# Kernel tuning notes

Hardware: AMD Instinct MI355X
Metric: run time of the kernel (lower is better)

The kernel has to match this reference:

```python
import jax, jax.numpy as jnp
import numpy as np

B, S, C, HD = 2, 4096, 2048, 128
H = C // HD  # 16 heads
EPS = 1.1920929e-07  # torch RMSNorm default eps for float32 (finfo.eps)


def _make_rope(seq_len, head_dim):
    # Standard RoPE 2x2 rotation matrices: [1, S, 1, head_dim//2, 2, 2]
    half = head_dim // 2
    freqs = 1.0 / (10000.0 ** (np.arange(0, half, dtype=np.float32) / half))
    ang = np.arange(seq_len, dtype=np.float32)[:, None] * freqs[None, :]  # [S, half]
    cos, sin = np.cos(ang), np.sin(ang)
    rot = np.stack([np.stack([cos, -sin], axis=-1),
                    np.stack([sin, cos], axis=-1)], axis=-2)  # [S, half, 2, 2]
    return jnp.asarray(rot[None, :, None])  # [1, S, 1, half, 2, 2]


def setup_inputs() -> dict:
    key = jax.random.key(0)
    ks = jax.random.split(key, 9)
    sc = 1.0 / np.sqrt(C)
    return {
        "x": jax.random.normal(ks[0], (B, S, C), jnp.float32),
        "rope": _make_rope(S, HD),
        "wq": jax.random.normal(ks[1], (C, C), jnp.float32) * sc,
        "bq": jax.random.normal(ks[2], (C,), jnp.float32) * 0.01,
        "wk": jax.random.normal(ks[3], (C, C), jnp.float32) * sc,
        "bk": jax.random.normal(ks[4], (C,), jnp.float32) * 0.01,
        "wv": jax.random.normal(ks[5], (C, C), jnp.float32) * sc,
        "bv": jax.random.normal(ks[6], (C,), jnp.float32) * 0.01,
        "q_norm_w": jnp.ones((HD,), jnp.float32),
        "k_norm_w": jnp.ones((HD,), jnp.float32),
    }


def _rmsnorm(t, w):
    t32 = t.astype(jnp.float32)
    inv = jax.lax.rsqrt(jnp.mean(t32 * t32, axis=-1, keepdims=True) + EPS)
    return (t32 * inv * w).astype(t.dtype)


def _apply_rotary(t, rope):
    # t: [B, S, H, HD] -> pairs [B, S, H, HD//2, 1, 2]; rope: [1, S, 1, HD//2, 2, 2]
    t32 = t.reshape(*t.shape[:-1], HD // 2, 1, 2).astype(jnp.float32)
    out = (rope * t32).sum(axis=-1)  # [B, S, H, HD//2, 2]
    return out.reshape(t.shape).astype(t.dtype)


def reference(x, rope, wq, bq, wk, bk, wv, bv, q_norm_w, k_norm_w):
    # QKV projections (torch Linear: x @ W^T + b)
    q = (jnp.einsum('bsc,oc->bso', x, wq) + bq).reshape(B, S, H, HD)
    k = (jnp.einsum('bsc,oc->bso', x, wk) + bk).reshape(B, S, H, HD)
    v = (jnp.einsum('bsc,oc->bso', x, wv) + bv).reshape(B, S, H, HD)
    # Per-head RMSNorm on q, k (in float32, cast back), then rotary
    q = _apply_rotary(_rmsnorm(q, q_norm_w), rope)
    k = _apply_rotary(_rmsnorm(k, k_norm_w), rope)
    return (q, k, v)
```

## Files before the change

kernel.cpp:

```cpp
#include <hip/hip_runtime.h>


#define M_DIM 8192
#define N_DIM 6144
#define K_DIM 2048
#define NKT 32
#define EPS_RMS 1.1920929e-07f

typedef __bf16 bf16x8 __attribute__((ext_vector_type(8)));
typedef float f32x4 __attribute__((ext_vector_type(4)));

__device__ __forceinline__ void gload16(const void* g, void* l) {
  __builtin_amdgcn_global_load_lds(
      (const __attribute__((address_space(1))) unsigned int*)g,
      (__attribute__((address_space(3))) unsigned int*)l, 16, 0, 0);
}

__device__ __forceinline__ unsigned short f2bf(float f) {
  union { float f; unsigned u; } x; x.f = f;
  unsigned r = x.u + 0x7FFFu + ((x.u >> 16) & 1u);
  return (unsigned short)(r >> 16);
}

__global__ void __launch_bounds__(256) cvt_all(
    const float* __restrict__ x, const float* __restrict__ wq,
    const float* __restrict__ wk, const float* __restrict__ wv,
    unsigned short* __restrict__ xbf, unsigned short* __restrict__ wbf) {
  const int nx4 = M_DIM * K_DIM / 4;
  const int nw4 = K_DIM * K_DIM / 4;
  const int tot = nx4 + 3 * nw4;
  int i = blockIdx.x * blockDim.x + threadIdx.x;
  const int stride = gridDim.x * blockDim.x;
  for (; i < tot; i += stride) {
    const float* s;
    unsigned short* d;
    int j;
    if (i < nx4) { s = x; d = xbf; j = i; }
    else {
      const int k = i - nx4;
      const int sel = k / nw4;
      j = k - sel * nw4;
      s = sel == 0 ? wq : (sel == 1 ? wk : wv);
      d = wbf + (size_t)sel * K_DIM * K_DIM;
    }
    const float4 v = reinterpret_cast<const float4*>(s)[j];
    ushort4 o;
    o.x = f2bf(v.x); o.y = f2bf(v.y); o.z = f2bf(v.z); o.w = f2bf(v.w);
    reinterpret_cast<ushort4*>(d)[j] = o;
  }
}

#define LDS4(ARR, BASE, OFF) (*(const f32x4*)((const char*)(ARR) + (BASE) + (OFF)))

#define SGB_DS(N)   __builtin_amdgcn_sched_group_barrier(0x100, (N), 0)
#define SGB_MFMA(N) __builtin_amdgcn_sched_group_barrier(0x8, (N), 0)

#define MFMA_PH(MH, NH)                                                              \
  {                                                                                  \
    _Pragma("unroll")                                                                \
    for (int mf4 = 0; mf4 < 4; ++mf4) {                                              \
      _Pragma("unroll")                                                              \
      for (int nf2 = 0; nf2 < 2; ++nf2) {                                            \
        f32x4& c = acc[(MH) * 4 + mf4][(NH) * 2 + nf2];                              \
        c = __builtin_amdgcn_mfma_f32_16x16x32_bf16(                                 \
            __builtin_bit_cast(bf16x8, Af[mf4][0]),                                  \
            __builtin_bit_cast(bf16x8, Bf[NH][nf2][0]), c, 0, 0, 0);                 \
        c = __builtin_amdgcn_mfma_f32_16x16x32_bf16(                                 \
            __builtin_bit_cast(bf16x8, Af[mf4][1]),                                  \
            __builtin_bit_cast(bf16x8, Bf[NH][nf2][1]), c, 0, 0, 0);                 \
      }                                                                              \
    }                                                                                \
  }

#define FENCE asm volatile("" ::: "memory")

__global__ void __launch_bounds__(512, 2) gemm_fused(
    const unsigned short* __restrict__ xbf, const unsigned short* __restrict__ wbf,
    const float* __restrict__ rope,
    const float* __restrict__ bq, const float* __restrict__ bk, const float* __restrict__ bv,
    const float* __restrict__ qnw, const float* __restrict__ knw,
    float* __restrict__ dout) {
  const int id = blockIdx.x;
  const int xcd = id & 7;
  const int jb = id >> 3;
  const int bm = (xcd << 2) | (jb & 3);
  const int bn = jb >> 2;
  const int m0 = bm << 8, n0 = bn << 8;
  const int tid = threadIdx.x;
  const int w = tid >> 6, l = tid & 63;
  const int l15 = l & 15, lhi = l >> 4;
  const int wr = w >> 2, wc = w & 3;

  __shared__ __align__(16) unsigned short As[32768];
  __shared__ __align__(16) unsigned short Bs[32768];

  const int srow = tid >> 3;
  const int schunk = (tid & 7) ^ (srow & 7);
  const unsigned short* aSrc = xbf + ((size_t)(m0 + srow) << 11) + (schunk << 3);
  const unsigned short* bSrc = wbf + ((size_t)(n0 + srow) << 11) + (schunk << 3);
  char* aDst = (char*)As + (w << 10);
  char* bDst = (char*)Bs + (w << 10);

#define STA(KT, Q) gload16(aSrc + ((size_t)(Q) << 17) + ((KT) << 6), aDst + ((((KT) & 1) << 15) + ((Q) << 13)))
#define STB(KT, Q) gload16(bSrc + ((size_t)(Q) << 17) + ((KT) << 6), bDst + ((((KT) & 1) << 15) + ((Q) << 13)))

  const int sl0 = ((lhi ^ (l15 & 7)) << 4);
  const int sl1 = (((lhi + 4) ^ (l15 & 7)) << 4);
  unsigned a0 = (wr << 14) + (l15 << 7) + sl0;
  unsigned a1 = (wr << 14) + (l15 << 7) + sl1;
  unsigned b0 = (wc << 13) + (l15 << 7) + sl0;
  unsigned b1 = (wc << 13) + (l15 << 7) + sl1;

  f32x4 acc[8][4];
#pragma unroll
  for (int i = 0; i < 8; ++i)
#pragma unroll
    for (int jj = 0; jj < 4; ++jj) acc[i][jj] = (f32x4){0.f, 0.f, 0.f, 0.f};

  f32x4 Af[4][2];
  f32x4 Bf[2][2][2];

  STA(0, 0); STA(0, 2);
  STB(0, 0); STB(0, 1); STB(0, 2); STB(0, 3);
  STA(0, 1); STA(0, 3);
  asm volatile("s_waitcnt vmcnt(2)" ::: "memory");
  __builtin_amdgcn_s_barrier();
  FENCE;

  for (int kt = 0; kt < NKT; ++kt) {
    const bool notLast = (kt < NKT - 1);
    Af[0][0] = LDS4(As, a0, 0);        Af[0][1] = LDS4(As, a1, 0);
    Bf[0][0][0] = LDS4(Bs, b0, 0);     Bf[0][0][1] = LDS4(Bs, b1, 0);
    Bf[0][1][0] = LDS4(Bs, b0, 2048);  Bf[0][1][1] = LDS4(Bs, b1, 2048);
    Af[1][0] = LDS4(As, a0, 2048);     Af[1][1] = LDS4(As, a1, 2048);
    Af[2][0] = LDS4(As, a0, 4096);     Af[2][1] = LDS4(As, a1, 4096);
    Af[3][0] = LDS4(As, a0, 6144);     Af[3][1] = LDS4(As, a1, 6144);
    Bf[1][0][0] = LDS4(Bs, b0, 4096);  Bf[1][0][1] = LDS4(Bs, b1, 4096);
    Bf[1][1][0] = LDS4(Bs, b0, 6144);  Bf[1][1][1] = LDS4(Bs, b1, 6144);
    if (notLast) {
      STA(kt + 1, 0); STA(kt + 1, 2);
      STB(kt + 1, 0); STB(kt + 1, 1); STB(kt + 1, 2); STB(kt + 1, 3);
    }
    __builtin_amdgcn_s_setprio(1);
    MFMA_PH(0, 0);
    MFMA_PH(0, 1);
    SGB_DS(4);  SGB_MFMA(2);
    SGB_DS(2);  SGB_MFMA(2);
    SGB_DS(2);  SGB_MFMA(4);
    SGB_DS(2);  SGB_MFMA(4);
    SGB_DS(2);  SGB_MFMA(4);
    SGB_DS(4);  SGB_MFMA(16);
    __builtin_amdgcn_s_setprio(0);
    if (notLast) { asm volatile("s_waitcnt vmcnt(6)" ::: "memory"); }
    else         { asm volatile("s_waitcnt vmcnt(0)" ::: "memory"); }
    __builtin_amdgcn_s_barrier();
    FENCE;
    Af[0][0] = LDS4(As, a0, 8192);  Af[0][1] = LDS4(As, a1, 8192);
    Af[1][0] = LDS4(As, a0, 10240); Af[1][1] = LDS4(As, a1, 10240);
    Af[2][0] = LDS4(As, a0, 12288); Af[2][1] = LDS4(As, a1, 12288);
    Af[3][0] = LDS4(As, a0, 14336); Af[3][1] = LDS4(As, a1, 14336);
    if (notLast) { STA(kt + 1, 1); STA(kt + 1, 3); }
    __builtin_amdgcn_s_setprio(1);
    MFMA_PH(1, 0);
    MFMA_PH(1, 1);
    SGB_DS(2);  SGB_MFMA(4);
    SGB_DS(2);  SGB_MFMA(4);
    SGB_DS(2);  SGB_MFMA(4);
    SGB_DS(2);  SGB_MFMA(4);
    SGB_MFMA(16);
    __builtin_amdgcn_s_setprio(0);
    if (notLast) { asm volatile("s_waitcnt vmcnt(2)" ::: "memory"); }
    __builtin_amdgcn_s_barrier();
    FENCE;
    a0 ^= 32768u; a1 ^= 32768u; b0 ^= 32768u; b1 ^= 32768u;
  }

  float* scr = (float*)As;
  const int sec = bn >> 3;
  const int nsec = (n0 & 2047) + (wc << 6);
  const float* bias = sec == 0 ? bq : (sec == 1 ? bk : bv);
  float biasv[4];
#pragma unroll
  for (int nf = 0; nf < 4; ++nf) biasv[nf] = bias[nsec + nf * 16 + l15];
  const size_t outBase = ((size_t)sec << 24);

  if (sec < 2) {
    const float* nwp = sec ? knw : qnw;
    const int colh = (wc & 1) << 6;
    float nwv[4];
#pragma unroll
    for (int nf = 0; nf < 4; ++nf) nwv[nf] = nwp[colh + nf * 16 + l15];
    float ssv[8][4];
#pragma unroll
    for (int mf = 0; mf < 8; ++mf) {
#pragma unroll
      for (int jj = 0; jj < 4; ++jj) {
        float ss = 0.f;
#pragma unroll
        for (int nf = 0; nf < 4; ++nf) {
          const float t = acc[mf][nf][jj] + biasv[nf];
          ss += t * t;
        }
        ss += __shfl_xor(ss, 1);
        ss += __shfl_xor(ss, 2);
        ss += __shfl_xor(ss, 4);
        ss += __shfl_xor(ss, 8);
        ssv[mf][jj] = ss;
      }
    }
    if (l15 == 0) {
#pragma unroll
      for (int mf = 0; mf < 8; ++mf)
#pragma unroll
        for (int jj = 0; jj < 4; ++jj)
          scr[(w << 7) + mf * 16 + (lhi << 2) + jj] = ssv[mf][jj];
    }
    __syncthreads();
#pragma unroll
    for (int mf = 0; mf < 8; ++mf) {
#pragma unroll
      for (int jj = 0; jj < 4; ++jj) {
        const float tot = ssv[mf][jj] + scr[((w ^ 1) << 7) + mf * 16 + (lhi << 2) + jj];
        const float inv = rsqrtf(tot * (1.0f / 128.0f) + EPS_RMS);
        const int m = m0 + (wr << 7) + mf * 16 + (lhi << 2) + jj;
        const float* rp = rope + ((size_t)(m & 4095) << 8);
        float* orow = dout + outBase + ((size_t)m << 11) + nsec + l15;
#pragma unroll
        for (int nf = 0; nf < 4; ++nf) {
          const float tn = (acc[mf][nf][jj] + biasv[nf]) * inv * nwv[nf];
          const float pn = __shfl_xor(tn, 1);
          const int ch = colh + nf * 16 + l15;
          const int jr = ch >> 1;
          const float o = fmaf(rp[jr << 2], tn, rp[(jr << 2) + 1 + (ch & 1)] * pn);
          orow[nf << 4] = o;
        }
      }
    }
  } else {
#pragma unroll
    for (int mf = 0; mf < 8; ++mf)
#pragma unroll
      for (int jj = 0; jj < 4; ++jj) {
        const int m = m0 + (wr << 7) + mf * 16 + (lhi << 2) + jj;
        float* orow = dout + outBase + ((size_t)m << 11) + nsec + l15;
#pragma unroll
        for (int nf = 0; nf < 4; ++nf) orow[nf << 4] = acc[mf][nf][jj] + biasv[nf];
      }
  }
}

extern "C" void kernel_launch(void* const* d_in, const int* in_sizes, int n_in,
                              void* d_out, int out_size, void* d_ws, size_t ws_size,
                              hipStream_t stream) {
  const float* x = (const float*)d_in[0];
  const float* rope = (const float*)d_in[1];
  const float* wq = (const float*)d_in[2];
  const float* bq = (const float*)d_in[3];
  const float* wk = (const float*)d_in[4];
  const float* bk = (const float*)d_in[5];
  const float* wv = (const float*)d_in[6];
  const float* bv = (const float*)d_in[7];
  const float* qnw = (const float*)d_in[8];
  const float* knw = (const float*)d_in[9];

  unsigned short* xbf = (unsigned short*)d_ws;
  unsigned short* wbf = xbf + (size_t)M_DIM * K_DIM;

  cvt_all<<<2048, 256, 0, stream>>>(x, wq, wk, wv, xbf, wbf);

  gemm_fused<<<(M_DIM / 256) * (N_DIM / 256), 512, 0, stream>>>(
      xbf, wbf, rope, bq, bk, bv, qnw, knw, (float*)d_out);
}
```

Baseline: 234.1 us.

## Split GEMM tile across 16 waves with 64x64 per-wave subtiles

Doubles the block to 1024 threads so each of 16 waves computes a 64x64 subtile of the unchanged 256x256 block tile, using 16 MFMA accumulators instead of 32. The LDS staging layout changes to two K-halves of 32 elements with a new swizzle, and the epilogue indexing is adjusted to match. The aim is more waves to hide latency and lower per-wave register pressure. In exchange, each wave reuses fewer loaded operands per MFMA, so LDS read traffic rises. The launch-bounds hint may also squeeze the VGPR budget enough to cause spills.

```diff
diff --git a/kernel.cpp b/kernel.cpp
--- a/kernel.cpp
+++ b/kernel.cpp
@@ -55,26 +55,22 @@
 #define SGB_DS(N)   __builtin_amdgcn_sched_group_barrier(0x100, (N), 0)
 #define SGB_MFMA(N) __builtin_amdgcn_sched_group_barrier(0x8, (N), 0)
 
-#define MFMA_PH(MH, NH)                                                              \
+#define MFMA_KS()                                                                    \
   {                                                                                  \
     _Pragma("unroll")                                                                \
-    for (int mf4 = 0; mf4 < 4; ++mf4) {                                              \
+    for (int mf = 0; mf < 4; ++mf) {                                                 \
       _Pragma("unroll")                                                              \
-      for (int nf2 = 0; nf2 < 2; ++nf2) {                                            \
-        f32x4& c = acc[(MH) * 4 + mf4][(NH) * 2 + nf2];                              \
-        c = __builtin_amdgcn_mfma_f32_16x16x32_bf16(                                 \
-            __builtin_bit_cast(bf16x8, Af[mf4][0]),                                  \
-            __builtin_bit_cast(bf16x8, Bf[NH][nf2][0]), c, 0, 0, 0);                 \
-        c = __builtin_amdgcn_mfma_f32_16x16x32_bf16(                                 \
-            __builtin_bit_cast(bf16x8, Af[mf4][1]),                                  \
-            __builtin_bit_cast(bf16x8, Bf[NH][nf2][1]), c, 0, 0, 0);                 \
+      for (int nf = 0; nf < 4; ++nf) {                                               \
+        acc[mf][nf] = __builtin_amdgcn_mfma_f32_16x16x32_bf16(                       \
+            __builtin_bit_cast(bf16x8, Af[mf]),                                      \
+            __builtin_bit_cast(bf16x8, Bf[nf]), acc[mf][nf], 0, 0, 0);               \
       }                                                                              \
     }                                                                                \
   }
 
 #define FENCE asm volatile("" ::: "memory")
 
-__global__ void __launch_bounds__(512, 2) gemm_fused(
+__global__ void __launch_bounds__(1024, 4) gemm_fused(
     const unsigned short* __restrict__ xbf, const unsigned short* __restrict__ wbf,
     const float* __restrict__ rope,
     const float* __restrict__ bq, const float* __restrict__ bk, const float* __restrict__ bv,
@@ -94,85 +90,66 @@
   __shared__ __align__(16) unsigned short As[32768];
   __shared__ __align__(16) unsigned short Bs[32768];
 
-  const int srow = tid >> 3;
-  const int schunk = (tid & 7) ^ (srow & 7);
-  const unsigned short* aSrc = xbf + ((size_t)(m0 + srow) << 11) + (schunk << 3);
-  const unsigned short* bSrc = wbf + ((size_t)(n0 + srow) << 11) + (schunk << 3);
+  const int srow = tid >> 2;
+  const int sch = (tid & 3) ^ ((tid >> 3) & 3);
+  const unsigned short* aSrc = xbf + ((size_t)(m0 + srow) << 11) + (sch << 3);
+  const unsigned short* bSrc = wbf + ((size_t)(n0 + srow) << 11) + (sch << 3);
   char* aDst = (char*)As + (w << 10);
   char* bDst = (char*)Bs + (w << 10);
 
-#define STA(KT, Q) gload16(aSrc + ((size_t)(Q) << 17) + ((KT) << 6), aDst + ((((KT) & 1) << 15) + ((Q) << 13)))
-#define STB(KT, Q) gload16(bSrc + ((size_t)(Q) << 17) + ((KT) << 6), bDst + ((((KT) & 1) << 15) + ((Q) << 13)))
-
-  const int sl0 = ((lhi ^ (l15 & 7)) << 4);
-  const int sl1 = (((lhi + 4) ^ (l15 & 7)) << 4);
-  unsigned a0 = (wr << 14) + (l15 << 7) + sl0;
-  unsigned a1 = (wr << 14) + (l15 << 7) + sl1;
-  unsigned b0 = (wc << 13) + (l15 << 7) + sl0;
-  unsigned b1 = (wc << 13) + (l15 << 7) + sl1;
-
-  f32x4 acc[8][4];
-#pragma unroll
-  for (int i = 0; i < 8; ++i)
+#define STAK(KT, KS) gload16(aSrc + ((KT) << 6) + ((KS) << 5), aDst + ((((KT) & 1) << 15) + ((KS) << 14)))
+#define STBK(KT, KS) gload16(bSrc + ((KT) << 6) + ((KS) << 5), bDst + ((((KT) & 1) << 15) + ((KS) << 14)))
+
+  const int slot = lhi ^ ((l15 >> 1) & 3);
+  unsigned aRd = (wr << 12) + (l15 << 6) + (slot << 4);
+  unsigned bRd = (wc << 12) + (l15 << 6) + (slot << 4);
+
+  f32x4 acc[4][4];
+#pragma unroll
+  for (int i = 0; i < 4; ++i)
 #pragma unroll
     for (int jj = 0; jj < 4; ++jj) acc[i][jj] = (f32x4){0.f, 0.f, 0.f, 0.f};
 
-  f32x4 Af[4][2];
-  f32x4 Bf[2][2][2];
-
-  STA(0, 0); STA(0, 2);
-  STB(0, 0); STB(0, 1); STB(0, 2); STB(0, 3);
-  STA(0, 1); STA(0, 3);
+  f32x4 Af[4], Bf[4];
+
+  STAK(0, 0); STBK(0, 0);
+  STAK(0, 1); STBK(0, 1);
   asm volatile("s_waitcnt vmcnt(2)" ::: "memory");
   __builtin_amdgcn_s_barrier();
   FENCE;
 
   for (int kt = 0; kt < NKT; ++kt) {
-    const bool notLast = (kt < NKT - 1);
-    Af[0][0] = LDS4(As, a0, 0);        Af[0][1] = LDS4(As, a1, 0);
-    Bf[0][0][0] = LDS4(Bs, b0, 0);     Bf[0][0][1] = LDS4(Bs, b1, 0);
-    Bf[0][1][0] = LDS4(Bs, b0, 2048);  Bf[0][1][1] = LDS4(Bs, b1, 2048);
-    Af[1][0] = LDS4(As, a0, 2048);     Af[1][1] = LDS4(As, a1, 2048);
-    Af[2][0] = LDS4(As, a0, 4096);     Af[2][1] = LDS4(As, a1, 4096);
-    Af[3][0] = LDS4(As, a0, 6144);     Af[3][1] = LDS4(As, a1, 6144);
-    Bf[1][0][0] = LDS4(Bs, b0, 4096);  Bf[1][0][1] = LDS4(Bs, b1, 4096);
-    Bf[1][1][0] = LDS4(Bs, b0, 6144);  Bf[1][1][1] = LDS4(Bs, b1, 6144);
-    if (notLast) {
-      STA(kt + 1, 0); STA(kt + 1, 2);
-      STB(kt + 1, 0); STB(kt + 1, 1); STB(kt + 1, 2); STB(kt + 1, 3);
-    }
+    const bool nl = (kt < NKT - 1);
+    Af[0] = LDS4(As, aRd, 0);    Bf[0] = LDS4(Bs, bRd, 0);
+    Af[1] = LDS4(As, aRd, 1024); Bf[1] = LDS4(Bs, bRd, 1024);
+    Af[2] = LDS4(As, aRd, 2048); Bf[2] = LDS4(Bs, bRd, 2048);
+    Af[3] = LDS4(As, aRd, 3072); Bf[3] = LDS4(Bs, bRd, 3072);
+    if (nl) { STAK(kt + 1, 0); STBK(kt + 1, 0); }
     __builtin_amdgcn_s_setprio(1);
-    MFMA_PH(0, 0);
-    MFMA_PH(0, 1);
-    SGB_DS(4);  SGB_MFMA(2);
-    SGB_DS(2);  SGB_MFMA(2);
-    SGB_DS(2);  SGB_MFMA(4);
-    SGB_DS(2);  SGB_MFMA(4);
-    SGB_DS(2);  SGB_MFMA(4);
-    SGB_DS(4);  SGB_MFMA(16);
+    MFMA_KS();
+    SGB_DS(4); SGB_MFMA(2);
+    SGB_DS(2); SGB_MFMA(1);
+    SGB_DS(2); SGB_MFMA(13);
     __builtin_amdgcn_s_setprio(0);
-    if (notLast) { asm volatile("s_waitcnt vmcnt(6)" ::: "memory"); }
-    else         { asm volatile("s_waitcnt vmcnt(0)" ::: "memory"); }
+    if (nl) { asm volatile("s_waitcnt vmcnt(2)" ::: "memory"); }
+    else    { asm volatile("s_waitcnt vmcnt(0)" ::: "memory"); }
     __builtin_amdgcn_s_barrier();
     FENCE;
-    Af[0][0] = LDS4(As, a0, 8192);  Af[0][1] = LDS4(As, a1, 8192);
-    Af[1][0] = LDS4(As, a0, 10240); Af[1][1] = LDS4(As, a1, 10240);
-    Af[2][0] = LDS4(As, a0, 12288); Af[2][1] = LDS4(As, a1, 12288);
-    Af[3][0] = LDS4(As, a0, 14336); Af[3][1] = LDS4(As, a1, 14336);
-    if (notLast) { STA(kt + 1, 1); STA(kt + 1, 3); }
+    Af[0] = LDS4(As, aRd, 16384); Bf[0] = LDS4(Bs, bRd, 16384);
+    Af[1] = LDS4(As, aRd, 17408); Bf[1] = LDS4(Bs, bRd, 17408);
+    Af[2] = LDS4(As, aRd, 18432); Bf[2] = LDS4(Bs, bRd, 18432);
+    Af[3] = LDS4(As, aRd, 19456); Bf[3] = LDS4(Bs, bRd, 19456);
+    if (nl) { STAK(kt + 1, 1); STBK(kt + 1, 1); }
     __builtin_amdgcn_s_setprio(1);
-    MFMA_PH(1, 0);
-    MFMA_PH(1, 1);
-    SGB_DS(2);  SGB_MFMA(4);
-    SGB_DS(2);  SGB_MFMA(4);
-    SGB_DS(2);  SGB_MFMA(4);
-    SGB_DS(2);  SGB_MFMA(4);
-    SGB_MFMA(16);
+    MFMA_KS();
+    SGB_DS(4); SGB_MFMA(2);
+    SGB_DS(2); SGB_MFMA(1);
+    SGB_DS(2); SGB_MFMA(13);
     __builtin_amdgcn_s_setprio(0);
-    if (notLast) { asm volatile("s_waitcnt vmcnt(2)" ::: "memory"); }
+    if (nl) { asm volatile("s_waitcnt vmcnt(2)" ::: "memory"); }
     __builtin_amdgcn_s_barrier();
     FENCE;
-    a0 ^= 32768u; a1 ^= 32768u; b0 ^= 32768u; b1 ^= 32768u;
+    aRd ^= 32768u; bRd ^= 32768u;
   }
 
   float* scr = (float*)As;
@@ -190,9 +167,9 @@
     float nwv[4];
 #pragma unroll
     for (int nf = 0; nf < 4; ++nf) nwv[nf] = nwp[colh + nf * 16 + l15];
-    float ssv[8][4];
-#pragma unroll
-    for (int mf = 0; mf < 8; ++mf) {
+    float ssv[4][4];
+#pragma unroll
+    for (int mf = 0; mf < 4; ++mf) {
 #pragma unroll
       for (int jj = 0; jj < 4; ++jj) {
         float ss = 0.f;
@@ -210,19 +187,19 @@
     }
     if (l15 == 0) {
 #pragma unroll
-      for (int mf = 0; mf < 8; ++mf)
+      for (int mf = 0; mf < 4; ++mf)
 #pragma unroll
         for (int jj = 0; jj < 4; ++jj)
-          scr[(w << 7) + mf * 16 + (lhi << 2) + jj] = ssv[mf][jj];
+          scr[(w << 6) + (mf << 4) + (lhi << 2) + jj] = ssv[mf][jj];
     }
     __syncthreads();
 #pragma unroll
-    for (int mf = 0; mf < 8; ++mf) {
+    for (int mf = 0; mf < 4; ++mf) {
 #pragma unroll
       for (int jj = 0; jj < 4; ++jj) {
-        const float tot = ssv[mf][jj] + scr[((w ^ 1) << 7) + mf * 16 + (lhi << 2) + jj];
+        const float tot = ssv[mf][jj] + scr[((w ^ 1) << 6) + (mf << 4) + (lhi << 2) + jj];
         const float inv = rsqrtf(tot * (1.0f / 128.0f) + EPS_RMS);
-        const int m = m0 + (wr << 7) + mf * 16 + (lhi << 2) + jj;
+        const int m = m0 + (wr << 6) + (mf << 4) + (lhi << 2) + jj;
         const float* rp = rope + ((size_t)(m & 4095) << 8);
         float* orow = dout + outBase + ((size_t)m << 11) + nsec + l15;
 #pragma unroll
@@ -238,10 +215,10 @@
     }
   } else {
 #pragma unroll
-    for (int mf = 0; mf < 8; ++mf)
+    for (int mf = 0; mf < 4; ++mf)
 #pragma unroll
       for (int jj = 0; jj < 4; ++jj) {
-        const int m = m0 + (wr << 7) + mf * 16 + (lhi << 2) + jj;
+        const int m = m0 + (wr << 6) + (mf << 4) + (lhi << 2) + jj;
         float* orow = dout + outBase + ((size_t)m << 11) + nsec + l15;
 #pragma unroll
         for (int nf = 0; nf < 4; ++nf) orow[nf << 4] = acc[mf][nf][jj] + biasv[nf];
@@ -268,6 +245,6 @@
 
   cvt_all<<<2048, 256, 0, stream>>>(x, wq, wk, wv, xbf, wbf);
 
-  gemm_fused<<<(M_DIM / 256) * (N_DIM / 256), 512, 0, stream>>>(
+  gemm_fused<<<(M_DIM / 256) * (N_DIM / 256), 1024, 0, stream>>>(
       xbf, wbf, rope, bq, bk, bv, qnw, knw, (float*)d_out);
 }
```

Result: slower. 242.6 us (+3.7%).

## Restructure GEMM main loop into four barrier-separated MFMA phases

Applied to the files above, without the earlier changes.

Replaces the two-phase main loop, which relied on sched_group_barrier interleaving, with four phases. Each phase issues its LDS fragment reads and part of the next-tile global-to-LDS loads, then does a block barrier, a full lgkmcnt wait and a sched_barrier before its MFMA block. Global loads for the next K tile are spread across the phases and B is issued before A. The aim is a ping-pong style schedule with more even overlap of memory and MFMA work, at the cost of extra barriers per K iteration and the loss of fine-grained compiler interleaving.

```diff
diff --git a/kernel.cpp b/kernel.cpp
--- a/kernel.cpp
+++ b/kernel.cpp
@@ -52,9 +52,6 @@
 
 #define LDS4(ARR, BASE, OFF) (*(const f32x4*)((const char*)(ARR) + (BASE) + (OFF)))
 
-#define SGB_DS(N)   __builtin_amdgcn_sched_group_barrier(0x100, (N), 0)
-#define SGB_MFMA(N) __builtin_amdgcn_sched_group_barrier(0x8, (N), 0)
-
 #define MFMA_PH(MH, NH)                                                              \
   {                                                                                  \
     _Pragma("unroll")                                                                \
@@ -73,6 +70,15 @@
   }
 
 #define FENCE asm volatile("" ::: "memory")
+
+#define PHASE_MFMA(MH, NH)                          \
+  FENCE;                                            \
+  __builtin_amdgcn_s_barrier();                     \
+  asm volatile("s_waitcnt lgkmcnt(0)" ::: "memory");\
+  __builtin_amdgcn_sched_barrier(0);                \
+  __builtin_amdgcn_s_setprio(1);                    \
+  MFMA_PH(MH, NH);                                  \
+  __builtin_amdgcn_s_setprio(0);
 
 __global__ void __launch_bounds__(512, 2) gemm_fused(
     const unsigned short* __restrict__ xbf, const unsigned short* __restrict__ wbf,
@@ -120,56 +126,41 @@
   f32x4 Af[4][2];
   f32x4 Bf[2][2][2];
 
+  STB(0, 0); STB(0, 1); STB(0, 2); STB(0, 3);
   STA(0, 0); STA(0, 2);
-  STB(0, 0); STB(0, 1); STB(0, 2); STB(0, 3);
   STA(0, 1); STA(0, 3);
   asm volatile("s_waitcnt vmcnt(2)" ::: "memory");
   __builtin_amdgcn_s_barrier();
   FENCE;
 
   for (int kt = 0; kt < NKT; ++kt) {
-    const bool notLast = (kt < NKT - 1);
+    const bool nl = (kt < NKT - 1);
     Af[0][0] = LDS4(As, a0, 0);        Af[0][1] = LDS4(As, a1, 0);
-    Bf[0][0][0] = LDS4(Bs, b0, 0);     Bf[0][0][1] = LDS4(Bs, b1, 0);
-    Bf[0][1][0] = LDS4(Bs, b0, 2048);  Bf[0][1][1] = LDS4(Bs, b1, 2048);
     Af[1][0] = LDS4(As, a0, 2048);     Af[1][1] = LDS4(As, a1, 2048);
     Af[2][0] = LDS4(As, a0, 4096);     Af[2][1] = LDS4(As, a1, 4096);
     Af[3][0] = LDS4(As, a0, 6144);     Af[3][1] = LDS4(As, a1, 6144);
+    Bf[0][0][0] = LDS4(Bs, b0, 0);     Bf[0][0][1] = LDS4(Bs, b1, 0);
+    Bf[0][1][0] = LDS4(Bs, b0, 2048);  Bf[0][1][1] = LDS4(Bs, b1, 2048);
+    if (nl) { STB(kt + 1, 0); STB(kt + 1, 1); }
+    PHASE_MFMA(0, 0);
+    __builtin_amdgcn_s_barrier();
     Bf[1][0][0] = LDS4(Bs, b0, 4096);  Bf[1][0][1] = LDS4(Bs, b1, 4096);
     Bf[1][1][0] = LDS4(Bs, b0, 6144);  Bf[1][1][1] = LDS4(Bs, b1, 6144);
-    if (notLast) {
-      STA(kt + 1, 0); STA(kt + 1, 2);
-      STB(kt + 1, 0); STB(kt + 1, 1); STB(kt + 1, 2); STB(kt + 1, 3);
-    }
-    __builtin_amdgcn_s_setprio(1);
-    MFMA_PH(0, 0);
-    MFMA_PH(0, 1);
-    SGB_DS(4);  SGB_MFMA(2);
-    SGB_DS(2);  SGB_MFMA(2);
-    SGB_DS(2);  SGB_MFMA(4);
-    SGB_DS(2);  SGB_MFMA(4);
-    SGB_DS(2);  SGB_MFMA(4);
-    SGB_DS(4);  SGB_MFMA(16);
-    __builtin_amdgcn_s_setprio(0);
-    if (notLast) { asm volatile("s_waitcnt vmcnt(6)" ::: "memory"); }
-    else         { asm volatile("s_waitcnt vmcnt(0)" ::: "memory"); }
-    __builtin_amdgcn_s_barrier();
-    FENCE;
+    if (nl) { STB(kt + 1, 2); STB(kt + 1, 3); }
+    PHASE_MFMA(0, 1);
+    if (nl) { asm volatile("s_waitcnt vmcnt(4)" ::: "memory"); }
+    else    { asm volatile("s_waitcnt vmcnt(0)" ::: "memory"); }
+    __builtin_amdgcn_s_barrier();
     Af[0][0] = LDS4(As, a0, 8192);  Af[0][1] = LDS4(As, a1, 8192);
     Af[1][0] = LDS4(As, a0, 10240); Af[1][1] = LDS4(As, a1, 10240);
     Af[2][0] = LDS4(As, a0, 12288); Af[2][1] = LDS4(As, a1, 12288);
     Af[3][0] = LDS4(As, a0, 14336); Af[3][1] = LDS4(As, a1, 14336);
-    if (notLast) { STA(kt + 1, 1); STA(kt + 1, 3); }
-    __builtin_amdgcn_s_setprio(1);
-    MFMA_PH(1, 0);
-    MFMA_PH(1, 1);
-    SGB_DS(2);  SGB_MFMA(4);
-    SGB_DS(2);  SGB_MFMA(4);
-    SGB_DS(2);  SGB_MFMA(4);
-    SGB_DS(2);  SGB_MFMA(4);
-    SGB_MFMA(16);
-    __builtin_amdgcn_s_setprio(0);
-    if (notLast) { asm volatile("s_waitcnt vmcnt(2)" ::: "memory"); }
+    if (nl) { STA(kt + 1, 0); STA(kt + 1, 2); }
+    PHASE_MFMA(1, 1);
+    __builtin_amdgcn_s_barrier();
+    if (nl) { STA(kt + 1, 1); STA(kt + 1, 3); }
+    PHASE_MFMA(1, 0);
+    if (nl) { asm volatile("s_waitcnt vmcnt(2)" ::: "memory"); }
     __builtin_amdgcn_s_barrier();
     FENCE;
     a0 ^= 32768u; a1 ^= 32768u; b0 ^= 32768u; b1 ^= 32768u;
```

Result: slower. 241.5 us (+3.2%).
